# Kernel optimization log

Measured on AMD Instinct MI355X. Metric: run time of the kernel, lower is better.

## Reference

```python
import jax, jax.numpy as jnp
import numpy as np

B, L, F = 512, 30, 64
N_LEADERS, MAX_LAG = 500, 10
H, TOP_K = 64, 5
SCALE = float(H) ** 0.5


def setup_inputs() -> dict:
    key = jax.random.key(0)
    ks = jax.random.split(key, 16)
    s = 0.05
    return {
        "target_seq": jax.random.normal(ks[0], (B, L, F), jnp.float32),
        "leader_raw_features": jax.random.normal(ks[1], (B, N_LEADERS, MAX_LAG, F), jnp.float32),
        # LSTM params (torch gate order i,f,g,o)
        "W_ih": jax.random.normal(ks[2], (4 * H, F), jnp.float32) * s,
        "W_hh": jax.random.normal(ks[3], (4 * H, H), jnp.float32) * s,
        "b_ih": jax.random.normal(ks[4], (4 * H,), jnp.float32) * s,
        "b_hh": jax.random.normal(ks[5], (4 * H,), jnp.float32) * s,
        # attention projections (bias-free)
        "W_Q": jax.random.normal(ks[6], (H, H), jnp.float32) * s,
        "W_K": jax.random.normal(ks[7], (H, F), jnp.float32) * s,
        # predictor MLP: F->H, H->H//2, H//2->1
        "Wp1": jax.random.normal(ks[8], (H, F), jnp.float32) * s,
        "bp1": jax.random.normal(ks[9], (H,), jnp.float32) * s,
        "Wp2": jax.random.normal(ks[10], (H // 2, H), jnp.float32) * s,
        "bp2": jax.random.normal(ks[11], (H // 2,), jnp.float32) * s,
        "Wp3": jax.random.normal(ks[12], (1, H // 2), jnp.float32) * s,
        "bp3": jax.random.normal(ks[13], (1,), jnp.float32) * s,
    }


def _lstm_last_hidden(x, W_ih, W_hh, b_ih, b_hh):
    # x: [B, L, F] -> last hidden state [B, H]
    b = x.shape[0]
    h0 = jnp.zeros((b, W_hh.shape[1]), x.dtype)

    def step(carry, xt):
        h, c = carry
        gates = xt @ W_ih.T + h @ W_hh.T + b_ih + b_hh  # [B, 4H]
        i, f, g, o = jnp.split(gates, 4, axis=-1)
        i = jax.nn.sigmoid(i)
        f = jax.nn.sigmoid(f)
        g = jnp.tanh(g)
        o = jax.nn.sigmoid(o)
        c = f * c + i * g
        h = o * jnp.tanh(c)
        return (h, c), None

    (h_last, _), _ = jax.lax.scan(step, (h0, h0), jnp.swapaxes(x, 0, 1))
    return h_last


def reference(target_seq, leader_raw_features, W_ih, W_hh, b_ih, b_hh,
              W_Q, W_K, Wp1, bp1, Wp2, bp2, Wp3, bp3):
    b = target_seq.shape[0]
    n_leaders, max_lag, feat = leader_raw_features.shape[1:]

    h_last = _lstm_last_hidden(target_seq, W_ih, W_hh, b_ih, b_hh)  # [B,H]
    query = h_last @ W_Q.T  # [B,H]

    # attn[b,n,l] = sum_h query[b,h] * (W_K @ raw[b,n,l])_h, fused to avoid
    # materializing the [B,N,LAG,H] key tensor.
    attn = jnp.einsum('bnlf,hf,bh->bnl', leader_raw_features, W_K, query) / SCALE

    flat_attn = attn.reshape(b, n_leaders * max_lag)
    k = min(TOP_K, flat_attn.shape[1])
    top_values, top_idx = jax.lax.top_k(flat_attn, k)  # [B,k]
    leader_idx = top_idx // max_lag
    lag_idx = top_idx % max_lag
    top_k_indices = jnp.stack([leader_idx, lag_idx], axis=-1)  # [B,k,2]
    top_k_scores = jax.nn.softmax(top_values, axis=-1)  # [B,k]

    raw_flat = leader_raw_features.reshape(b, n_leaders * max_lag, feat)
    selected = jnp.take_along_axis(raw_flat, top_idx[:, :, None], axis=1)  # [B,k,F]
    weighted = jnp.einsum('bkf,bk->bf', selected, top_k_scores)  # [B,F]

    # predictor MLP (dropout is identity in eval)
    h1 = jax.nn.relu(weighted @ Wp1.T + bp1)
    h2 = jax.nn.relu(h1 @ Wp2.T + bp2)
    pred = h2 @ Wp3.T + bp3  # [B,1]
    return pred, top_k_indices, top_k_scores, attn
```

## Files before the change

### kernel.cpp

```cpp
#include <hip/hip_runtime.h>
#include <math.h>

#define B_SZ   512
#define L_SEQ  30
#define F_DIM  64
#define N_LEAD 500
#define MAXLAG 10
#define H_DIM  64
#define NROWS  5000
#define TOPK   5

#define OFF_IDX   512
#define OFF_SCORE 5632
#define OFF_ATTN  8192

__global__ __launch_bounds__(256) void lstm_kq_kernel(
    const float* __restrict__ x,
    const float* __restrict__ W_ih,
    const float* __restrict__ W_hh,
    const float* __restrict__ b_ih,
    const float* __restrict__ b_hh,
    const float* __restrict__ W_Q,
    const float* __restrict__ W_K,
    float* __restrict__ kq)
{
    __shared__ float xs[L_SEQ * F_DIM];
    __shared__ float hs[H_DIM];
    __shared__ float gates[256];

    const int b = blockIdx.x;
    const int t = threadIdx.x;

    for (int i = t; i < L_SEQ * F_DIM; i += 256)
        xs[i] = x[b * L_SEQ * F_DIM + i];
    if (t < H_DIM) hs[t] = 0.f;

    float4 wih[16], whh[16];
    const float4* wihp = (const float4*)(W_ih + t * 64);
    const float4* whhp = (const float4*)(W_hh + t * 64);
#pragma unroll
    for (int k = 0; k < 16; ++k) { wih[k] = wihp[k]; whh[k] = whhp[k]; }
    const float bsum = b_ih[t] + b_hh[t];

    float c = 0.f;
    __syncthreads();

    for (int step = 0; step < L_SEQ; ++step) {
        float g = bsum;
        const float4* xv = (const float4*)(xs + step * F_DIM);
        const float4* hv = (const float4*)hs;
#pragma unroll
        for (int k = 0; k < 16; ++k) {
            float4 xk = xv[k], hk = hv[k];
            g += wih[k].x * xk.x + wih[k].y * xk.y + wih[k].z * xk.z + wih[k].w * xk.w;
            g += whh[k].x * hk.x + whh[k].y * hk.y + whh[k].z * hk.z + whh[k].w * hk.w;
        }
        gates[t] = g;
        __syncthreads();
        if (t < H_DIM) {
            float ig = 1.f / (1.f + expf(-gates[t]));
            float fg = 1.f / (1.f + expf(-gates[t + 64]));
            float gg = tanhf(gates[t + 128]);
            float og = 1.f / (1.f + expf(-gates[t + 192]));
            c = fg * c + ig * gg;
            hs[t] = og * tanhf(c);
        }
        __syncthreads();
    }

    if (t < H_DIM) {
        float q = 0.f;
        const float4* wq = (const float4*)(W_Q + t * 64);
        const float4* hv = (const float4*)hs;
#pragma unroll
        for (int k = 0; k < 16; ++k) {
            float4 w = wq[k], h4 = hv[k];
            q += w.x * h4.x + w.y * h4.y + w.z * h4.z + w.w * h4.w;
        }
        gates[t] = q;
    }
    __syncthreads();
    if (t < F_DIM) {
        float acc = 0.f;
        for (int h = 0; h < H_DIM; ++h)
            acc += gates[h] * W_K[h * F_DIM + t];
        kq[b * F_DIM + t] = acc;
    }
}

#define CHUNKS 10
#define ROWS_PER_BLK 500
__global__ __launch_bounds__(256) void attn_kernel(
    const float4* __restrict__ raw,
    const float* __restrict__ kq,
    float* __restrict__ attn)
{
    const int b     = blockIdx.x / CHUNKS;
    const int chunk = blockIdx.x % CHUNKS;
    const int sub   = threadIdx.x & 15;
    const int rg    = threadIdx.x >> 4;

    const float4 kqv = ((const float4*)(kq + b * 64))[sub];
    const int base   = chunk * ROWS_PER_BLK;
    const long rowb  = (long)b * NROWS;

    for (int it = 0; it < 8; ++it) {
#pragma unroll
        for (int j = 0; j < 4; ++j) {
            int row = base + it * 64 + j * 16 + rg;
            if (row < base + ROWS_PER_BLK) {
                float4 v = raw[(rowb + row) * 16 + sub];
                float s = v.x * kqv.x + v.y * kqv.y + v.z * kqv.z + v.w * kqv.w;
                s += __shfl_xor(s, 8);
                s += __shfl_xor(s, 4);
                s += __shfl_xor(s, 2);
                s += __shfl_xor(s, 1);
                if (sub == 0) attn[rowb + row] = s * 0.125f;
            }
        }
    }
}

__global__ __launch_bounds__(256) void topk_mlp_kernel(
    const float* __restrict__ attn,
    const float* __restrict__ raw,
    const float* __restrict__ Wp1, const float* __restrict__ bp1,
    const float* __restrict__ Wp2, const float* __restrict__ bp2,
    const float* __restrict__ Wp3, const float* __restrict__ bp3,
    float* __restrict__ out)
{
    __shared__ float av[NROWS];
    __shared__ float redv[4];
    __shared__ int   redi[4];
    __shared__ float topv[TOPK];
    __shared__ int   topi[TOPK];
    __shared__ float sc[TOPK];
    __shared__ float wsum[64];
    __shared__ float h1[64];
    __shared__ float h2[32];

    const int b = blockIdx.x, t = threadIdx.x;

    for (int i = t; i < NROWS; i += 256) av[i] = attn[(long)b * NROWS + i];
    __syncthreads();

    for (int p = 0; p < TOPK; ++p) {
        float bv = -INFINITY; int bi = 0x7fffffff;
        for (int i = t; i < NROWS; i += 256) {
            float v = av[i];
            if (v > bv || (v == bv && i < bi)) { bv = v; bi = i; }
        }
#pragma unroll
        for (int m = 32; m >= 1; m >>= 1) {
            float ov = __shfl_xor(bv, m);
            int   oi = __shfl_xor(bi, m);
            if (ov > bv || (ov == bv && oi < bi)) { bv = ov; bi = oi; }
        }
        if ((t & 63) == 0) { redv[t >> 6] = bv; redi[t >> 6] = bi; }
        __syncthreads();
        if (t == 0) {
            for (int w = 1; w < 4; ++w)
                if (redv[w] > bv || (redv[w] == bv && redi[w] < bi)) { bv = redv[w]; bi = redi[w]; }
            topv[p] = bv; topi[p] = bi;
            av[bi] = -INFINITY;
        }
        __syncthreads();
    }

    if (t == 0) {
        float mx = topv[0];
        float e[TOPK], s = 0.f;
        for (int k = 0; k < TOPK; ++k) { e[k] = expf(topv[k] - mx); s += e[k]; }
        float inv = 1.f / s;
        for (int k = 0; k < TOPK; ++k) {
            sc[k] = e[k] * inv;
            out[OFF_IDX + b * 10 + 2 * k]     = (float)(topi[k] / MAXLAG);
            out[OFF_IDX + b * 10 + 2 * k + 1] = (float)(topi[k] % MAXLAG);
            out[OFF_SCORE + b * TOPK + k]     = sc[k];
        }
    }
    __syncthreads();

    if (t < 64) {
        float acc = 0.f;
        for (int k = 0; k < TOPK; ++k)
            acc += sc[k] * raw[((long)b * NROWS + topi[k]) * 64 + t];
        wsum[t] = acc;
    }
    __syncthreads();
    if (t < 64) {
        float a = bp1[t];
        for (int f = 0; f < 64; ++f) a += Wp1[t * 64 + f] * wsum[f];
        h1[t] = fmaxf(a, 0.f);
    }
    __syncthreads();
    if (t < 32) {
        float a = bp2[t];
        for (int f = 0; f < 64; ++f) a += Wp2[t * 64 + f] * h1[f];
        h2[t] = fmaxf(a, 0.f);
    }
    __syncthreads();
    if (t == 0) {
        float a = bp3[0];
        for (int f = 0; f < 32; ++f) a += Wp3[f] * h2[f];
        out[b] = a;
    }
}

extern "C" void kernel_launch(void* const* d_in, const int* in_sizes, int n_in,
                              void* d_out, int out_size, void* d_ws, size_t ws_size,
                              hipStream_t stream) {
    const float* target = (const float*)d_in[0];
    const float* raw    = (const float*)d_in[1];
    const float* W_ih   = (const float*)d_in[2];
    const float* W_hh   = (const float*)d_in[3];
    const float* b_ih   = (const float*)d_in[4];
    const float* b_hh   = (const float*)d_in[5];
    const float* W_Q    = (const float*)d_in[6];
    const float* W_K    = (const float*)d_in[7];
    const float* Wp1    = (const float*)d_in[8];
    const float* bp1    = (const float*)d_in[9];
    const float* Wp2    = (const float*)d_in[10];
    const float* bp2    = (const float*)d_in[11];
    const float* Wp3    = (const float*)d_in[12];
    const float* bp3    = (const float*)d_in[13];

    float* out      = (float*)d_out;
    float* kq       = (float*)d_ws;
    float* attn_out = out + OFF_ATTN;

    hipLaunchKernelGGL(lstm_kq_kernel, dim3(B_SZ), dim3(256), 0, stream,
                       target, W_ih, W_hh, b_ih, b_hh, W_Q, W_K, kq);
    hipLaunchKernelGGL(attn_kernel, dim3(B_SZ * CHUNKS), dim3(256), 0, stream,
                       (const float4*)raw, kq, attn_out);
    hipLaunchKernelGGL(topk_mlp_kernel, dim3(B_SZ), dim3(256), 0, stream,
                       attn_out, raw, Wp1, bp1, Wp2, bp2, Wp3, bp3, out);
}
```

Before: 202.5 us.

## Fuse attention scoring into top-k/MLP kernel and speed up LSTM recurrence

Merges the attention-score kernel into the top-k/MLP kernel, so each 512-thread block computes its batch's 5000 scores into shared memory while also writing them to the output. This drops one launch and the global round-trip re-read of the attention scores. Each thread now computes a full 64-wide row dot product with kq held in scalar registers, replacing the shuffle reduction. The LSTM kernel uses fast exp-based sigmoid and tanh and precomputes the input projection for the next step off the critical path. The trade-offs are parallelism (512 blocks instead of 5120 for the bandwidth-heavy scan) and slightly lower accuracy of the activations.

Result: slower. 207.2 us (+2.3%).

```diff
diff --git a/kernel.cpp b/kernel.cpp
--- a/kernel.cpp
+++ b/kernel.cpp
@@ -13,6 +13,32 @@
 #define OFF_IDX   512
 #define OFF_SCORE 5632
 #define OFF_ATTN  8192
+
+__device__ __forceinline__ float fast_sigmoid(float x) {
+    return 1.f / (1.f + __expf(-x));
+}
+__device__ __forceinline__ float fast_tanh(float x) {
+    float ax = fabsf(x);
+    float t  = __expf(-2.f * ax);
+    float r  = (1.f - t) / (1.f + t);
+    return copysignf(r, x);
+}
+__device__ __forceinline__ float sfl(float v) {
+    return __uint_as_float(__builtin_amdgcn_readfirstlane(__float_as_uint(v)));
+}
+
+__device__ __forceinline__ float dot16(const float4* __restrict__ w,
+                                       const float4* __restrict__ v) {
+    float a0 = 0.f, a1 = 0.f, a2 = 0.f, a3 = 0.f;
+#pragma unroll
+    for (int k = 0; k < 16; k += 4) {
+        a0 += w[k+0].x*v[k+0].x + w[k+0].y*v[k+0].y + w[k+0].z*v[k+0].z + w[k+0].w*v[k+0].w;
+        a1 += w[k+1].x*v[k+1].x + w[k+1].y*v[k+1].y + w[k+1].z*v[k+1].z + w[k+1].w*v[k+1].w;
+        a2 += w[k+2].x*v[k+2].x + w[k+2].y*v[k+2].y + w[k+2].z*v[k+2].z + w[k+2].w*v[k+2].w;
+        a3 += w[k+3].x*v[k+3].x + w[k+3].y*v[k+3].y + w[k+3].z*v[k+3].z + w[k+3].w*v[k+3].w;
+    }
+    return (a0 + a1) + (a2 + a3);
+}
 
 __global__ __launch_bounds__(256) void lstm_kq_kernel(
     const float* __restrict__ x,
@@ -24,9 +50,9 @@
     const float* __restrict__ W_K,
     float* __restrict__ kq)
 {
-    __shared__ float xs[L_SEQ * F_DIM];
-    __shared__ float hs[H_DIM];
-    __shared__ float gates[256];
+    __shared__ __align__(16) float xs[L_SEQ * F_DIM];
+    __shared__ __align__(16) float hs[H_DIM];
+    __shared__ __align__(16) float gates[256];
 
     const int b = blockIdx.x;
     const int t = threadIdx.x;
@@ -45,108 +71,94 @@
     float c = 0.f;
     __syncthreads();
 
+    float gx = bsum + dot16(wih, (const float4*)xs);
+
     for (int step = 0; step < L_SEQ; ++step) {
-        float g = bsum;
-        const float4* xv = (const float4*)(xs + step * F_DIM);
-        const float4* hv = (const float4*)hs;
-#pragma unroll
-        for (int k = 0; k < 16; ++k) {
-            float4 xk = xv[k], hk = hv[k];
-            g += wih[k].x * xk.x + wih[k].y * xk.y + wih[k].z * xk.z + wih[k].w * xk.w;
-            g += whh[k].x * hk.x + whh[k].y * hk.y + whh[k].z * hk.z + whh[k].w * hk.w;
-        }
+        float g = gx + dot16(whh, (const float4*)hs);
         gates[t] = g;
         __syncthreads();
         if (t < H_DIM) {
-            float ig = 1.f / (1.f + expf(-gates[t]));
-            float fg = 1.f / (1.f + expf(-gates[t + 64]));
-            float gg = tanhf(gates[t + 128]);
-            float og = 1.f / (1.f + expf(-gates[t + 192]));
+            float ig = fast_sigmoid(gates[t]);
+            float fg = fast_sigmoid(gates[t + 64]);
+            float gg = fast_tanh(gates[t + 128]);
+            float og = fast_sigmoid(gates[t + 192]);
             c = fg * c + ig * gg;
-            hs[t] = og * tanhf(c);
-        }
-        __syncthreads();
-    }
-
-    if (t < H_DIM) {
-        float q = 0.f;
-        const float4* wq = (const float4*)(W_Q + t * 64);
-        const float4* hv = (const float4*)hs;
-#pragma unroll
-        for (int k = 0; k < 16; ++k) {
-            float4 w = wq[k], h4 = hv[k];
-            q += w.x * h4.x + w.y * h4.y + w.z * h4.z + w.w * h4.w;
-        }
-        gates[t] = q;
-    }
+            hs[t] = og * fast_tanh(c);
+        }
+        if (step + 1 < L_SEQ)
+            gx = bsum + dot16(wih, (const float4*)(xs + (step + 1) * F_DIM));
+        __syncthreads();
+    }
+
+    if (t < H_DIM)
+        gates[t] = dot16((const float4*)(W_Q + t * 64), (const float4*)hs);
     __syncthreads();
     if (t < F_DIM) {
-        float acc = 0.f;
-        for (int h = 0; h < H_DIM; ++h)
-            acc += gates[h] * W_K[h * F_DIM + t];
-        kq[b * F_DIM + t] = acc;
-    }
-}
-
-#define CHUNKS 10
-#define ROWS_PER_BLK 500
-__global__ __launch_bounds__(256) void attn_kernel(
-    const float4* __restrict__ raw,
+        float a0 = 0.f, a1 = 0.f;
+        for (int h = 0; h < H_DIM; h += 2) {
+            a0 += gates[h]     * W_K[h * F_DIM + t];
+            a1 += gates[h + 1] * W_K[(h + 1) * F_DIM + t];
+        }
+        kq[b * F_DIM + t] = a0 + a1;
+    }
+}
+
+__global__ __launch_bounds__(512, 8) void fused_attn_topk_kernel(
+    const float* __restrict__ raw,
     const float* __restrict__ kq,
-    float* __restrict__ attn)
-{
-    const int b     = blockIdx.x / CHUNKS;
-    const int chunk = blockIdx.x % CHUNKS;
-    const int sub   = threadIdx.x & 15;
-    const int rg    = threadIdx.x >> 4;
-
-    const float4 kqv = ((const float4*)(kq + b * 64))[sub];
-    const int base   = chunk * ROWS_PER_BLK;
-    const long rowb  = (long)b * NROWS;
-
-    for (int it = 0; it < 8; ++it) {
-#pragma unroll
-        for (int j = 0; j < 4; ++j) {
-            int row = base + it * 64 + j * 16 + rg;
-            if (row < base + ROWS_PER_BLK) {
-                float4 v = raw[(rowb + row) * 16 + sub];
-                float s = v.x * kqv.x + v.y * kqv.y + v.z * kqv.z + v.w * kqv.w;
-                s += __shfl_xor(s, 8);
-                s += __shfl_xor(s, 4);
-                s += __shfl_xor(s, 2);
-                s += __shfl_xor(s, 1);
-                if (sub == 0) attn[rowb + row] = s * 0.125f;
-            }
-        }
-    }
-}
-
-__global__ __launch_bounds__(256) void topk_mlp_kernel(
-    const float* __restrict__ attn,
-    const float* __restrict__ raw,
     const float* __restrict__ Wp1, const float* __restrict__ bp1,
     const float* __restrict__ Wp2, const float* __restrict__ bp2,
     const float* __restrict__ Wp3, const float* __restrict__ bp3,
     float* __restrict__ out)
 {
     __shared__ float av[NROWS];
-    __shared__ float redv[4];
-    __shared__ int   redi[4];
+    __shared__ float redv[8];
+    __shared__ int   redi[8];
     __shared__ float topv[TOPK];
     __shared__ int   topi[TOPK];
     __shared__ float sc[TOPK];
-    __shared__ float wsum[64];
-    __shared__ float h1[64];
+    __shared__ __align__(16) float wsum[64];
+    __shared__ __align__(16) float h1[64];
     __shared__ float h2[32];
 
     const int b = blockIdx.x, t = threadIdx.x;
 
-    for (int i = t; i < NROWS; i += 256) av[i] = attn[(long)b * NROWS + i];
-    __syncthreads();
-
-    for (int p = 0; p < TOPK; ++p) {
+    const float* kqp = kq + b * 64;
+#define LQ(i) const float q##i##x = sfl(kqp[4*(i)+0]), q##i##y = sfl(kqp[4*(i)+1]), \
+                          q##i##z = sfl(kqp[4*(i)+2]), q##i##w = sfl(kqp[4*(i)+3]);
+    LQ(0) LQ(1) LQ(2) LQ(3) LQ(4) LQ(5) LQ(6) LQ(7)
+    LQ(8) LQ(9) LQ(10) LQ(11) LQ(12) LQ(13) LQ(14) LQ(15)
+#undef LQ
+
+    float* attn_g = out + OFF_ATTN + (size_t)b * NROWS;
+    const float4* p = (const float4*)raw + ((size_t)b * NROWS + t) * 16;
+
+#define DOT4(acc, v, i) acc += v.x*q##i##x + v.y*q##i##y + v.z*q##i##z + v.w*q##i##w;
+#define BODY(r) { \
+    float4 v0=p[0],v1=p[1],v2=p[2],v3=p[3],v4=p[4],v5=p[5],v6=p[6],v7=p[7]; \
+    float s0=0.f,s1=0.f,s2=0.f,s3=0.f; \
+    DOT4(s0,v0,0) DOT4(s1,v1,1) DOT4(s2,v2,2) DOT4(s3,v3,3) \
+    DOT4(s0,v4,4) DOT4(s1,v5,5) DOT4(s2,v6,6) DOT4(s3,v7,7) \
+    v0=p[8];v1=p[9];v2=p[10];v3=p[11];v4=p[12];v5=p[13];v6=p[14];v7=p[15]; \
+    DOT4(s0,v0,8)  DOT4(s1,v1,9)  DOT4(s2,v2,10) DOT4(s3,v3,11) \
+    DOT4(s0,v4,12) DOT4(s1,v5,13) DOT4(s2,v6,14) DOT4(s3,v7,15) \
+    float s = ((s0+s1)+(s2+s3)) * 0.125f; \
+    av[r] = s; attn_g[r] = s; }
+
+    int r = t;
+#pragma unroll 1
+    for (int pass = 0; pass < 9; ++pass) {
+        BODY(r)
+        r += 512; p += 512 * 16;
+    }
+    if (r < NROWS) { BODY(r) }
+#undef BODY
+#undef DOT4
+    __syncthreads();
+
+    for (int pp = 0; pp < TOPK; ++pp) {
         float bv = -INFINITY; int bi = 0x7fffffff;
-        for (int i = t; i < NROWS; i += 256) {
+        for (int i = t; i < NROWS; i += 512) {
             float v = av[i];
             if (v > bv || (v == bv && i < bi)) { bv = v; bi = i; }
         }
@@ -159,9 +171,9 @@
         if ((t & 63) == 0) { redv[t >> 6] = bv; redi[t >> 6] = bi; }
         __syncthreads();
         if (t == 0) {
-            for (int w = 1; w < 4; ++w)
+            for (int w = 1; w < 8; ++w)
                 if (redv[w] > bv || (redv[w] == bv && redi[w] < bi)) { bv = redv[w]; bi = redi[w]; }
-            topv[p] = bv; topi[p] = bi;
+            topv[pp] = bv; topi[pp] = bi;
             av[bi] = -INFINITY;
         }
         __syncthreads();
@@ -170,8 +182,10 @@
     if (t == 0) {
         float mx = topv[0];
         float e[TOPK], s = 0.f;
-        for (int k = 0; k < TOPK; ++k) { e[k] = expf(topv[k] - mx); s += e[k]; }
+#pragma unroll
+        for (int k = 0; k < TOPK; ++k) { e[k] = __expf(topv[k] - mx); s += e[k]; }
         float inv = 1.f / s;
+#pragma unroll
         for (int k = 0; k < TOPK; ++k) {
             sc[k] = e[k] * inv;
             out[OFF_IDX + b * 10 + 2 * k]     = (float)(topi[k] / MAXLAG);
@@ -183,25 +197,35 @@
 
     if (t < 64) {
         float acc = 0.f;
+#pragma unroll
         for (int k = 0; k < TOPK; ++k)
-            acc += sc[k] * raw[((long)b * NROWS + topi[k]) * 64 + t];
+            acc += sc[k] * raw[((size_t)b * NROWS + topi[k]) * 64 + t];
         wsum[t] = acc;
     }
     __syncthreads();
     if (t < 64) {
         float a = bp1[t];
-        for (int f = 0; f < 64; ++f) a += Wp1[t * 64 + f] * wsum[f];
+        const float4* w = (const float4*)(Wp1 + t * 64);
+        const float4* v = (const float4*)wsum;
+#pragma unroll
+        for (int k = 0; k < 16; ++k)
+            a += w[k].x*v[k].x + w[k].y*v[k].y + w[k].z*v[k].z + w[k].w*v[k].w;
         h1[t] = fmaxf(a, 0.f);
     }
     __syncthreads();
     if (t < 32) {
         float a = bp2[t];
-        for (int f = 0; f < 64; ++f) a += Wp2[t * 64 + f] * h1[f];
+        const float4* w = (const float4*)(Wp2 + t * 64);
+        const float4* v = (const float4*)h1;
+#pragma unroll
+        for (int k = 0; k < 16; ++k)
+            a += w[k].x*v[k].x + w[k].y*v[k].y + w[k].z*v[k].z + w[k].w*v[k].w;
         h2[t] = fmaxf(a, 0.f);
     }
     __syncthreads();
     if (t == 0) {
         float a = bp3[0];
+#pragma unroll
         for (int f = 0; f < 32; ++f) a += Wp3[f] * h2[f];
         out[b] = a;
     }
@@ -225,14 +249,11 @@
     const float* Wp3    = (const float*)d_in[12];
     const float* bp3    = (const float*)d_in[13];
 
-    float* out      = (float*)d_out;
-    float* kq       = (float*)d_ws;
-    float* attn_out = out + OFF_ATTN;
+    float* out = (float*)d_out;
+    float* kq  = (float*)d_ws;
 
     hipLaunchKernelGGL(lstm_kq_kernel, dim3(B_SZ), dim3(256), 0, stream,
                        target, W_ih, W_hh, b_ih, b_hh, W_Q, W_K, kq);
-    hipLaunchKernelGGL(attn_kernel, dim3(B_SZ * CHUNKS), dim3(256), 0, stream,
-                       (const float4*)raw, kq, attn_out);
-    hipLaunchKernelGGL(topk_mlp_kernel, dim3(B_SZ), dim3(256), 0, stream,
-                       attn_out, raw, Wp1, bp1, Wp2, bp2, Wp3, bp3, out);
-}
+    hipLaunchKernelGGL(fused_attn_topk_kernel, dim3(B_SZ), dim3(512), 0, stream,
+                       raw, kq, Wp1, bp1, Wp2, bp2, Wp3, bp3, out);
+}
```
